# Performance work log

Hardware: AMD Instinct MI355X
Metric: run time of the kernel (lower is better)

The kernel has to match this reference:

```python
import jax, jax.numpy as jnp
import numpy as np

CDF = 0.9  # sparse_threshold


def setup_inputs() -> dict:
    key = jax.random.key(0)
    ks = jax.random.split(key, 8)
    BS, FPS, PPF, XC, K, YS = 8, 64, 1024, 64, 64, 128
    N = BS * FPS * PPF  # 524288 points
    x = jax.random.normal(ks[0], (N, XC), jnp.float32)
    # locations: cols 0,1 are spatial coords, col 2 is the (sorted) frame id;
    # uniform ragged structure: exactly PPF points per frame.
    frame_id = (jnp.arange(N, dtype=jnp.int32) // PPF)
    loc01 = jax.random.randint(ks[1], (N, 2), 0, 64, dtype=jnp.int32)
    locations = jnp.concatenate([loc01, frame_id[:, None]], axis=1)
    y = jax.random.normal(ks[2], (BS, YS), jnp.float32)
    Wc = jax.random.normal(ks[3], (K, XC), jnp.float32) * 0.05
    bc = jnp.zeros((K,), jnp.float32)
    Wy = jax.random.normal(ks[4], (K, YS), jnp.float32) * 0.05
    Wa = jax.random.normal(ks[5], (1, K), jnp.float32) * 0.05
    ba = jnp.zeros((1,), jnp.float32)
    return {"x": x, "locations": locations, "y": y, "Wc": Wc, "bc": bc,
            "Wy": Wy, "Wa": Wa, "ba": ba,
            "frames_per_sample": FPS, "points_per_frame": PPF}


def reference(x, locations, y, Wc, bc, Wy, Wa, ba, frames_per_sample, points_per_frame):
    N, XC = x.shape
    P = points_per_frame
    T = N // P                       # total frames = sum(x_lens)
    y_k = y @ Wy.T                   # [bs, k]   (y_affine, no bias)
    x_k = x @ Wc.T + bc              # [N, k]    (channel_affine)
    frame_id = locations[:, 2]       # [N]
    batch_id = frame_id // frames_per_sample  # which sample each point belongs to
    # attn_weight_affine(tanh(x_k + y_k[sample]))  -> [N]
    scores = (jnp.tanh(x_k + y_k[batch_id]) @ Wa.T + ba)[:, 0]
    w = jax.nn.softmax(scores.reshape(T, P), axis=-1)  # per-frame softmax
    # top-p (CDF) sparsification per frame: sort desc, cumsum < cdf, keep one more
    order = jnp.argsort(-w, axis=-1)                      # [T, P] desc order
    w_sorted = jnp.take_along_axis(w, order, axis=-1)
    csum = jnp.cumsum(w_sorted, axis=-1)
    keep = jnp.sum(csum < CDF, axis=-1) + 1               # mask[sum(mask)] = True
    rank = jnp.argsort(order, axis=-1)                    # inverse permutation
    mask = (rank < keep[:, None]).reshape(-1)             # [N] bool
    new_x = x[mask, :]
    new_locations = locations[mask, :]
    return new_x, new_locations
```

## Files before the change

### kernel.cpp

```cpp
#include <hip/hip_runtime.h>
#include <math.h>


typedef __attribute__((ext_vector_type(8))) short short8v;
typedef __attribute__((ext_vector_type(4))) float f32x4;

__device__ __forceinline__ unsigned short bf16rne(float f) {
    unsigned u = __builtin_bit_cast(unsigned, f);
    return (unsigned short)((u + 0x7fffu + ((u >> 16) & 1u)) >> 16);
}
__device__ __forceinline__ float bf16f(unsigned short h) {
    unsigned u = ((unsigned)h) << 16;
    return __builtin_bit_cast(float, u);
}

__device__ __forceinline__ float fast_tanh(float z) {
    float az = fabsf(z);
    float e  = __expf(-2.0f * az);
    float r  = (1.0f - e) * __builtin_amdgcn_rcpf(1.0f + e);
    return copysignf(r, z);
}

__global__ __launch_bounds__(512) void prep_kernel(const float* __restrict__ y,
                                                   const float* __restrict__ Wy,
                                                   const float* __restrict__ Wc,
                                                   const float* __restrict__ bc,
                                                   const float* __restrict__ Wa,
                                                   short8v* __restrict__ wfrag,
                                                   float* __restrict__ pre,
                                                   float* __restrict__ waCopy) {
    __shared__ float yks[512];
    const int tid = threadIdx.x;
    {
        const int b = tid >> 6, k = tid & 63;
        const float* yrow = y + b * 128;
        const float* wrow = Wy + k * 128;
        float a0 = 0.f, a1 = 0.f, a2 = 0.f, a3 = 0.f;
#pragma unroll
        for (int j = 0; j < 128; j += 4) {
            a0 += yrow[j + 0] * wrow[j + 0];
            a1 += yrow[j + 1] * wrow[j + 1];
            a2 += yrow[j + 2] * wrow[j + 2];
            a3 += yrow[j + 3] * wrow[j + 3];
        }
        yks[tid] = (a0 + a1) + (a2 + a3);
    }
    __syncthreads();

    for (int f = tid; f < 1536; f += 512) {
        int ln = f & 63, t = f >> 6, kt = t & 3, pc = t >> 2;
        int cs = pc & 1, pr = pc >> 1;
        int k = kt * 16 + (ln & 15), c = cs * 32 + 8 * (ln >> 4);
        const float* wr = Wc + k * 64 + c;
        short8v o;
#pragma unroll
        for (int j = 0; j < 8; ++j) {
            float v = wr[j];
            unsigned short hb = bf16rne(v);
            if (pr == 0) { o[j] = (short)hb; continue; }
            float r1 = v - bf16f(hb);
            unsigned short mb = bf16rne(r1);
            if (pr == 1) { o[j] = (short)mb; continue; }
            float r2 = r1 - bf16f(mb);
            o[j] = (short)bf16rne(r2);
        }
        wfrag[f] = o;
    }
    pre[tid] = bc[tid & 63] + yks[tid];
    if (tid < 64) waCopy[tid] = Wa[tid];
}

__global__ __launch_bounds__(256, 4) void score_kernel(const float* __restrict__ x,
                                                       const short8v* __restrict__ wfrag,
                                                       const float* __restrict__ pre,
                                                       const float* __restrict__ waCopy,
                                                       const float* __restrict__ ba,
                                                       float* __restrict__ scores) {
    __shared__ short8v sWf[1536];
    __shared__ float sPre[64];
    __shared__ float sWaS[64];
    const int tid  = threadIdx.x;
    const int lane = tid & 63;
    const int wv   = tid >> 6;
    const int b    = blockIdx.x >> 9;
    const int pbase = blockIdx.x * 128 + wv * 32;

    const int prow0 = pbase + (lane & 15);
    const int cg = 8 * (lane >> 4);
    float4 u[2][2][2];
#pragma unroll
    for (int pt = 0; pt < 2; ++pt) {
        const float* xr = x + (long long)(prow0 + pt * 16) * 64;
#pragma unroll
        for (int cs = 0; cs < 2; ++cs) {
            const float4* xp4 = (const float4*)(xr + cs * 32 + cg);
            u[pt][cs][0] = xp4[0];
            u[pt][cs][1] = xp4[1];
        }
    }

    for (int f = tid; f < 1536; f += 256) sWf[f] = wfrag[f];
    if (tid < 64) { sPre[tid] = pre[b * 64 + tid]; sWaS[tid] = waCopy[tid]; }
    __syncthreads();

    short8v A[2][3][2];
#pragma unroll
    for (int pt = 0; pt < 2; ++pt) {
#pragma unroll
        for (int cs = 0; cs < 2; ++cs) {
            float4 u0 = u[pt][cs][0], u1 = u[pt][cs][1];
            float v[8] = {u0.x, u0.y, u0.z, u0.w, u1.x, u1.y, u1.z, u1.w};
            short8v h, m, l;
#pragma unroll
            for (int j = 0; j < 8; ++j) {
                float vv = v[j];
                unsigned short hb = (unsigned short)(__builtin_bit_cast(unsigned, vv) >> 16);
                float r1 = vv - bf16f(hb);
                unsigned short mb = (unsigned short)(__builtin_bit_cast(unsigned, r1) >> 16);
                float r2 = r1 - bf16f(mb);
                unsigned short lb = (unsigned short)(__builtin_bit_cast(unsigned, r2) >> 16);
                h[j] = (short)hb; m[j] = (short)mb; l[j] = (short)lb;
            }
            A[pt][0][cs] = h; A[pt][1][cs] = m; A[pt][2][cs] = l;
        }
    }

    f32x4 sacc[2] = {{0.f, 0.f, 0.f, 0.f}, {0.f, 0.f, 0.f, 0.f}};
    const float ba0 = ba[0];
    const int kcol = lane & 15;
#pragma unroll
    for (int kt = 0; kt < 4; ++kt) {
        short8v B[3][2];
#pragma unroll
        for (int pr = 0; pr < 3; ++pr)
#pragma unroll
            for (int cs = 0; cs < 2; ++cs)
                B[pr][cs] = sWf[((pr * 2 + cs) * 4 + kt) * 64 + lane];
        const float prek = sPre[kt * 16 + kcol];
        const float wak = sWaS[kt * 16 + kcol];
#pragma unroll
        for (int pt = 0; pt < 2; ++pt) {
            f32x4 acc = {0.f, 0.f, 0.f, 0.f};
#pragma unroll
            for (int cs = 0; cs < 2; ++cs) {
                acc = __builtin_amdgcn_mfma_f32_16x16x32_bf16(A[pt][2][cs], B[0][cs], acc, 0, 0, 0);
                acc = __builtin_amdgcn_mfma_f32_16x16x32_bf16(A[pt][0][cs], B[2][cs], acc, 0, 0, 0);
                acc = __builtin_amdgcn_mfma_f32_16x16x32_bf16(A[pt][1][cs], B[1][cs], acc, 0, 0, 0);
                acc = __builtin_amdgcn_mfma_f32_16x16x32_bf16(A[pt][1][cs], B[0][cs], acc, 0, 0, 0);
                acc = __builtin_amdgcn_mfma_f32_16x16x32_bf16(A[pt][0][cs], B[1][cs], acc, 0, 0, 0);
                acc = __builtin_amdgcn_mfma_f32_16x16x32_bf16(A[pt][0][cs], B[0][cs], acc, 0, 0, 0);
            }
#pragma unroll
            for (int r = 0; r < 4; ++r) {
                float z = acc[r] + prek;
                sacc[pt][r] += wak * fast_tanh(z);
            }
        }
    }

#pragma unroll
    for (int pt = 0; pt < 2; ++pt)
#pragma unroll
        for (int r = 0; r < 4; ++r) {
            float v = sacc[pt][r];
            v += __shfl_xor(v, 1);
            v += __shfl_xor(v, 2);
            v += __shfl_xor(v, 4);
            v += __shfl_xor(v, 8);
            if (kcol == 0)
                scores[pbase + pt * 16 + (lane >> 4) * 4 + r] = v + ba0;
        }
}

__global__ __launch_bounds__(1024) void tile_kernel(const float* __restrict__ scores,
                                                    int* __restrict__ flags,
                                                    int* __restrict__ keepcnt) {
    const int t = blockIdx.x, tid = threadIdx.x;
    __shared__ float sw[1024];
    __shared__ int   si[1024];
    __shared__ float red[16];
    __shared__ int   keep_s;

    const int lane = tid & 63, wid = tid >> 6;
    float s = scores[t * 1024 + tid];

    float m = s;
#pragma unroll
    for (int o = 32; o; o >>= 1) m = fmaxf(m, __shfl_xor(m, o));
    if (lane == 0) red[wid] = m;
    __syncthreads();
    float mb = red[0];
#pragma unroll
    for (int q = 1; q < 16; ++q) mb = fmaxf(mb, red[q]);
    __syncthreads();

    float e = expf(s - mb);
    float su = e;
#pragma unroll
    for (int o = 32; o; o >>= 1) su += __shfl_xor(su, o);
    if (lane == 0) red[wid] = su;
    __syncthreads();
    float tot = 0.f;
#pragma unroll
    for (int q = 0; q < 16; ++q) tot += red[q];

    float w  = e / tot;
    int   idx = tid;

    for (int kk = 2; kk <= 1024; kk <<= 1) {
        for (int j = kk >> 1; j > 0; j >>= 1) {
            bool lower = (tid & j) == 0;
            bool desc2 = (tid & kk) == 0;
            float wp; int ip;
            if (j >= 64) {
                sw[tid] = w; si[tid] = idx;
                __syncthreads();
                wp = sw[tid ^ j]; ip = si[tid ^ j];
                bool before = (w > wp) || (w == wp && idx < ip);
                bool keep = desc2 ? (before == lower) : (before != lower);
                if (!keep) { w = wp; idx = ip; }
                __syncthreads();
            } else {
                wp = __shfl_xor(w, j);
                ip = __shfl_xor(idx, j);
                bool before = (w > wp) || (w == wp && idx < ip);
                bool keep = desc2 ? (before == lower) : (before != lower);
                if (!keep) { w = wp; idx = ip; }
            }
        }
    }

    sw[tid] = w;
    __syncthreads();

    if (tid == 0) {
        float c = 0.f; int kp = 0;
#pragma unroll 8
        for (int q = 0; q < 1024; ++q) { c += sw[q]; if (c < 0.9f) ++kp; }
        keep_s = kp + 1;
        keepcnt[t] = kp + 1;
    }
    __syncthreads();

    flags[t * 1024 + idx] = (tid < keep_s) ? 1 : 0;
}

__global__ __launch_bounds__(1024) void compact_kernel(const float* __restrict__ x,
                                                       const int* __restrict__ locs,
                                                       const int* __restrict__ flags,
                                                       const int* __restrict__ keepcnt,
                                                       float* __restrict__ out,
                                                       int M) {
    const int t = blockIdx.x, tid = threadIdx.x;
    const long long gi = (long long)t * 1024 + tid;
    const int f = flags[gi];
    const int lane = tid & 63, wid = tid >> 6;

    __shared__ int wtot[16];
    __shared__ int woff[16];
    __shared__ int rowsrc[1024];
    __shared__ int nk_s;
    __shared__ int base_s;

    if (wid == 0) {
        int s = 0;
#pragma unroll
        for (int j = 0; j < 8; ++j) {
            int q = lane * 8 + j;
            int kc = keepcnt[q];
            if (q < t) s += kc;
        }
#pragma unroll
        for (int o = 32; o; o >>= 1) s += __shfl_xor(s, o);
        if (lane == 0) base_s = s;
    }

    unsigned long long ball = __ballot(f != 0);
    int wpre = __popcll(ball & (((unsigned long long)1 << lane) - 1ULL));
    if (lane == 63) wtot[wid] = wpre + f;
    __syncthreads();
    if (tid == 0) {
        int r = 0;
#pragma unroll
        for (int q = 0; q < 16; ++q) { woff[q] = r; r += wtot[q]; }
        nk_s = r;
    }
    __syncthreads();

    const int base = base_s;
    if (f) {
        const int local = woff[wid] + wpre;
        rowsrc[local] = tid;
        const long long pos = (long long)base + local;
        float* lout = out + (long long)M * 64 + pos * 3;
        lout[0] = (float)locs[gi * 3 + 0];
        lout[1] = (float)locs[gi * 3 + 1];
        lout[2] = (float)locs[gi * 3 + 2];
    }
    __syncthreads();

    const int nk = nk_s;
    const int rsub = tid >> 4;
    const int col  = tid & 15;
    for (int r0 = 0; r0 < nk; r0 += 64) {
        const int rr = r0 + rsub;
        if (rr < nk) {
            const int srow = rowsrc[rr];
            const float4* src = (const float4*)(x + ((long long)t * 1024 + srow) * 64);
            float4* dst = (float4*)(out + (long long)(base + rr) * 64);
            dst[col] = src[col];
        }
    }
}

extern "C" void kernel_launch(void* const* d_in, const int* in_sizes, int n_in,
                              void* d_out, int out_size, void* d_ws, size_t ws_size,
                              hipStream_t stream) {
    const float* x    = (const float*)d_in[0];
    const int*   locs = (const int*)d_in[1];
    const float* y    = (const float*)d_in[2];
    const float* Wc   = (const float*)d_in[3];
    const float* bc   = (const float*)d_in[4];
    const float* Wy   = (const float*)d_in[5];
    const float* Wa   = (const float*)d_in[6];
    const float* ba   = (const float*)d_in[7];

    const int N = in_sizes[0] / 64;
    const int T = N / 1024;
    const int M = out_size / 67;

    float* ws      = (float*)d_ws;
    float* scores  = ws + 512;
    int*   flags   = (int*)(ws + 512 + N);
    int*   keepcnt = flags + N;
    int*   toffs   = keepcnt + T;
    short8v* wfrag = (short8v*)(ws + 512 + 2 * N + 2 * T);
    float* pre     = ws + 512 + 2 * N + 2 * T + 6144;
    float* waCopy  = pre + 512;
    (void)toffs;

    prep_kernel<<<1, 512, 0, stream>>>(y, Wy, Wc, bc, Wa, wfrag, pre, waCopy);
    score_kernel<<<N / 128, 256, 0, stream>>>(x, wfrag, pre, waCopy, ba, scores);
    tile_kernel<<<T, 1024, 0, stream>>>(scores, flags, keepcnt);
    compact_kernel<<<T, 1024, 0, stream>>>(x, locs, flags, keepcnt, (float*)d_out, M);
}
```

Baseline: 133.3 us.

## Fuse tile and compact kernels via cooperative grid sync

Merges the per-frame softmax/sort kernel and the compaction kernel into one cooperative kernel. Keep flags now live in shared memory instead of a global array, and a grid-wide sync makes every frame's keep count visible before prefix offsets are computed. This removes one kernel launch and the global flags round trip. In exchange it depends on cooperative launch residency: all 512 blocks of 1024 threads must be co-resident, and the grid sync adds its own cost.

```diff
diff --git a/kernel.cpp b/kernel.cpp
--- a/kernel.cpp
+++ b/kernel.cpp
@@ -1,5 +1,8 @@
 #include <hip/hip_runtime.h>
+#include <hip/hip_cooperative_groups.h>
 #include <math.h>
+
+namespace cg = cooperative_groups;
 
 
 typedef __attribute__((ext_vector_type(8))) short short8v;
@@ -172,14 +175,21 @@
         }
 }
 
-__global__ __launch_bounds__(1024) void tile_kernel(const float* __restrict__ scores,
-                                                    int* __restrict__ flags,
-                                                    int* __restrict__ keepcnt) {
+__global__ __launch_bounds__(1024, 8) void tile_compact_kernel(const float* __restrict__ scores,
+                                                               const float* __restrict__ x,
+                                                               const int* __restrict__ locs,
+                                                               int* __restrict__ keepcnt,
+                                                               float* __restrict__ out,
+                                                               int M) {
     const int t = blockIdx.x, tid = threadIdx.x;
     __shared__ float sw[1024];
     __shared__ int   si[1024];
+    __shared__ int   rowsrc[1024];
     __shared__ float red[16];
     __shared__ int   keep_s;
+    __shared__ int   base_s;
+    __shared__ int   wtot[16];
+    __shared__ int   woff[16];
 
     const int lane = tid & 63, wid = tid >> 6;
     float s = scores[t * 1024 + tid];
@@ -231,8 +241,8 @@
     }
 
     sw[tid] = w;
-    __syncthreads();
-
+    si[tid] = 0;
+    __syncthreads();
     if (tid == 0) {
         float c = 0.f; int kp = 0;
 #pragma unroll 8
@@ -242,39 +252,24 @@
     }
     __syncthreads();
 
-    flags[t * 1024 + idx] = (tid < keep_s) ? 1 : 0;
-}
-
-__global__ __launch_bounds__(1024) void compact_kernel(const float* __restrict__ x,
-                                                       const int* __restrict__ locs,
-                                                       const int* __restrict__ flags,
-                                                       const int* __restrict__ keepcnt,
-                                                       float* __restrict__ out,
-                                                       int M) {
-    const int t = blockIdx.x, tid = threadIdx.x;
-    const long long gi = (long long)t * 1024 + tid;
-    const int f = flags[gi];
-    const int lane = tid & 63, wid = tid >> 6;
-
-    __shared__ int wtot[16];
-    __shared__ int woff[16];
-    __shared__ int rowsrc[1024];
-    __shared__ int nk_s;
-    __shared__ int base_s;
+    if (tid < keep_s) si[idx] = 1;
+
+    cg::this_grid().sync();
 
     if (wid == 0) {
-        int s = 0;
+        int acc = 0;
 #pragma unroll
         for (int j = 0; j < 8; ++j) {
             int q = lane * 8 + j;
             int kc = keepcnt[q];
-            if (q < t) s += kc;
-        }
-#pragma unroll
-        for (int o = 32; o; o >>= 1) s += __shfl_xor(s, o);
-        if (lane == 0) base_s = s;
-    }
-
+            if (q < t) acc += kc;
+        }
+#pragma unroll
+        for (int o = 32; o; o >>= 1) acc += __shfl_xor(acc, o);
+        if (lane == 0) base_s = acc;
+    }
+
+    const int f = si[tid];
     unsigned long long ball = __ballot(f != 0);
     int wpre = __popcll(ball & (((unsigned long long)1 << lane) - 1ULL));
     if (lane == 63) wtot[wid] = wpre + f;
@@ -283,11 +278,11 @@
         int r = 0;
 #pragma unroll
         for (int q = 0; q < 16; ++q) { woff[q] = r; r += wtot[q]; }
-        nk_s = r;
     }
     __syncthreads();
 
     const int base = base_s;
+    const long long gi = (long long)t * 1024 + tid;
     if (f) {
         const int local = woff[wid] + wpre;
         rowsrc[local] = tid;
@@ -299,7 +294,7 @@
     }
     __syncthreads();
 
-    const int nk = nk_s;
+    const int nk = keep_s;
     const int rsub = tid >> 4;
     const int col  = tid & 15;
     for (int r0 = 0; r0 < nk; r0 += 64) {
@@ -327,20 +322,21 @@
 
     const int N = in_sizes[0] / 64;
     const int T = N / 1024;
-    const int M = out_size / 67;
+    int M = out_size / 67;
 
     float* ws      = (float*)d_ws;
     float* scores  = ws + 512;
-    int*   flags   = (int*)(ws + 512 + N);
-    int*   keepcnt = flags + N;
-    int*   toffs   = keepcnt + T;
+    int*   keepcnt = (int*)(ws + 512 + N);
     short8v* wfrag = (short8v*)(ws + 512 + 2 * N + 2 * T);
     float* pre     = ws + 512 + 2 * N + 2 * T + 6144;
     float* waCopy  = pre + 512;
-    (void)toffs;
 
     prep_kernel<<<1, 512, 0, stream>>>(y, Wy, Wc, bc, Wa, wfrag, pre, waCopy);
     score_kernel<<<N / 128, 256, 0, stream>>>(x, wfrag, pre, waCopy, ba, scores);
-    tile_kernel<<<T, 1024, 0, stream>>>(scores, flags, keepcnt);
-    compact_kernel<<<T, 1024, 0, stream>>>(x, locs, flags, keepcnt, (float*)d_out, M);
-}
+
+    float* out = (float*)d_out;
+    void* args[] = {(void*)&scores, (void*)&x, (void*)&locs,
+                    (void*)&keepcnt, (void*)&out, (void*)&M};
+    hipLaunchCooperativeKernel((const void*)tile_compact_kernel,
+                               dim3(T), dim3(1024), args, 0, stream);
+}
```

Measured after the change: 170.6 us. 1.28x slower.
